# Kernel tuning notes

Hardware: AMD Instinct MI355X
Metric: run time of the kernel (lower is better)

Reference implementation:

```python
import jax, jax.numpy as jnp
import numpy as np

NT, NS, NH, NG = 365, 1024, 64, 32
NW = NH * 8 + 2


def setup_inputs() -> dict:
    key = jax.random.key(0)
    k1, k2, k3, k4 = jax.random.split(key, 4)
    std = 1.0 / np.sqrt(NH)
    x = jax.random.normal(k1, (NT, NS, 4), dtype=jnp.float32)
    # make P (precip) nonnegative and T1 < T2 plausible-ish; math is still generic
    xc = jax.random.normal(k2, (NS, NG), dtype=jnp.float32)
    fc_w = jax.random.uniform(k3, (NW, NG), minval=-std, maxval=std, dtype=jnp.float32)
    fc_b = jax.random.uniform(k4, (NW,), minval=-std, maxval=std, dtype=jnp.float32)
    return {"x": x, "xc": xc, "fc_w": fc_w, "fc_b": fc_b}


def reference(x, xc, fc_w, fc_b):
    nh = NH
    P, E, T1, T2 = x[..., 0], x[..., 1], x[..., 2], x[..., 3]  # each [nt, ns]
    Ta = (T1 + T2) * 0.5
    # rain/snow partition: rP = 1 - arccos((T1+T2)/(T2-T1))/3.1415, masked
    valid = (T1 < 0) & (T2 > 0)
    denom = jnp.where(valid, T2 - T1, 1.0)
    ratio = jnp.clip(jnp.where(valid, (T1 + T2) / denom, 0.0), -0.999999, 0.999999)
    rP = 1.0 - jnp.arccos(ratio) / 3.1415
    rP = jnp.where(T1 >= 0, 1.0, rP)
    rP = jnp.where(T2 <= 0, 0.0, rP)
    Ps = (1.0 - rP) * P  # snow   [nt, ns]
    Pl = rP * P          # liquid [nt, ns]

    w = xc @ fc_w.T + fc_b  # [ns, nh*8+2]
    gm = jnp.exp(w[:, :nh]) + 1.0
    ge = jax.nn.sigmoid(w[:, nh:2 * nh]) * 2.0
    go = jax.nn.sigmoid(w[:, 2 * nh:3 * nh])
    gl = jnp.exp(w[:, 3 * nh:4 * nh] * 2.0)
    ga = jax.nn.softmax(w[:, 4 * nh:5 * nh], axis=1)  # Dropout in eval mode = identity
    gb = jax.nn.sigmoid(w[:, 5 * nh:6 * nh])
    qb = jax.nn.relu(w[:, -1]) / nh  # [ns]
    kb = jax.nn.sigmoid(w[:, 6 * nh:7 * nh]) / 10.0
    gi = jax.nn.sigmoid(w[:, 7 * nh:8 * nh])

    ns = P.shape[1]
    init = (jnp.zeros((ns, nh), jnp.float32),) * 3  # S0, H0, G0

    def step(carry, inp):
        S0, H0, G0 = carry
        Ps_k, Pl_k, Ta_k, E_k = inp  # each [ns]
        S = S0 + Ps_k[:, None]
        Sm = jnp.minimum(S0, jax.nn.relu(Ta_k[:, None] * gm))  # snowmelt
        H = jax.nn.relu(H0 + Sm + Pl_k[:, None] * gi - E_k[:, None] * ge)
        Q1 = jax.nn.relu(H - gl)
        Q2a = jnp.minimum(H, gl) * go
        Q2 = Q2a * (1.0 - gb)
        G = G0 + Q2a * gb
        Q3 = G * kb
        H0n = jnp.minimum(H - Q2a, gl)
        G0n = G - Q3
        S0n = S - Sm
        Y = jnp.sum((Q1 + Q2 + Q3 + qb[:, None]) * ga, axis=1)  # [ns]
        return (S0n, H0n, G0n), Y

    _, Yout = jax.lax.scan(step, init, (Ps, Pl, Ta, E))
    return Yout  # [nt, ns]
```

## Files before the change

kernel.cpp:

```cpp
#include <hip/hip_runtime.h>
#include <math.h>

#define NT_ 365
#define NS_ 1024
#define NH_ 64
#define NG_ 32
#define NW_ 514
#define CH_ 64
#define NCHUNK_ 6
#define YPAD_ 65
#define SUB_ 8

__device__ __forceinline__ float sigmoidf(float v) {
  return 1.0f / (1.0f + expf(-v));
}

__device__ __forceinline__ float4 compute_met(float4 xv) {
  const float P = xv.x, E = xv.y, T1 = xv.z, T2 = xv.w;
  const float Ta = (T1 + T2) * 0.5f;
  float rP;
  if (T2 <= 0.0f) {
    rP = 0.0f;
  } else if (T1 >= 0.0f) {
    rP = 1.0f;
  } else {
    float r = (T1 + T2) / (T2 - T1);
    r = fminf(fmaxf(r, -0.999999f), 0.999999f);
    rP = 1.0f - acosf(r) * (1.0f / 3.1415f);
  }
  float4 m;
  m.x = (1.0f - rP) * P;
  m.y = rP * P;
  m.z = fmaxf(Ta, 0.0f);
  m.w = E;
  return m;
}

__global__ __launch_bounds__(256) void waternet_scan(
    const float* __restrict__ x,
    const float* __restrict__ xc,
    const float* __restrict__ fc_w,
    const float* __restrict__ fc_b,
    float* __restrict__ out)
{
  __shared__ float4 smet[4][CH_];
  __shared__ float  ytile[4][CH_ * YPAD_];

  const int tid  = threadIdx.x;
  const int lane = tid & 63;
  const int wv   = tid >> 6;
  const int site = (blockIdx.x << 2) + wv;
  const int us   = __builtin_amdgcn_readfirstlane(site);
  const float4* xp = (const float4*)x;

  float4 xcur = xp[lane * NS_ + site];

  float acc[8];
#pragma unroll
  for (int k = 0; k < 8; ++k) acc[k] = fc_b[k * NH_ + lane];
  float accq = fc_b[NW_ - 1];

  const float4* xcq = (const float4*)(xc + us * NG_);
  const float4* wq4 = (const float4*)fc_w;
#pragma unroll
  for (int g4 = 0; g4 < NG_ / 4; ++g4) {
    const float4 xv = xcq[g4];
#pragma unroll
    for (int k = 0; k < 8; ++k) {
      const float4 w = wq4[(k * NH_ + lane) * (NG_ / 4) + g4];
      acc[k] = fmaf(xv.x, w.x, acc[k]);
      acc[k] = fmaf(xv.y, w.y, acc[k]);
      acc[k] = fmaf(xv.z, w.z, acc[k]);
      acc[k] = fmaf(xv.w, w.w, acc[k]);
    }
    {
      const float4 w = wq4[(NW_ - 1) * (NG_ / 4) + g4];
      accq = fmaf(xv.x, w.x, accq);
      accq = fmaf(xv.y, w.y, accq);
      accq = fmaf(xv.z, w.z, accq);
      accq = fmaf(xv.w, w.w, accq);
    }
  }

  const float gm = expf(acc[0]) + 1.0f;
  const float ge = sigmoidf(acc[1]) * 2.0f;
  const float go = sigmoidf(acc[2]);
  const float gl = expf(acc[3] * 2.0f);
  float mx = acc[4];
#pragma unroll
  for (int mm = 32; mm >= 1; mm >>= 1) mx = fmaxf(mx, __shfl_xor(mx, mm, 64));
  const float ex = expf(acc[4] - mx);
  float sm = ex;
#pragma unroll
  for (int mm = 32; mm >= 1; mm >>= 1) sm += __shfl_xor(sm, mm, 64);
  const float ga = ex / sm;
  const float gb = sigmoidf(acc[5]);
  const float kb = sigmoidf(acc[6]) * 0.1f;
  const float gi = sigmoidf(acc[7]);
  const float qb = fmaxf(accq, 0.0f) * (1.0f / NH_);
  const float kb1m = 1.0f - kb;
  const float nge  = -ge;
  const float gq1  = go * (1.0f - gb) - 1.0f;

  float S0 = 0.0f, H0 = 0.0f, G0 = 0.0f;

  smet[wv][lane] = compute_met(xcur);

  auto step = [&](const float4 mt, float* ywaddr) {
    const float melt = mt.z * gm;
    const float Sm   = fminf(S0, melt);
    const float base = H0 + Sm;
    S0 = (S0 - Sm) + mt.x;
    const float t3 = fmaf(mt.y, gi, base);
    const float H  = fmaxf(fmaf(mt.w, nge, t3), 0.0f);
    const float M  = fminf(H, gl);
    const float Q2a = M * go;
    H0 = fminf(H - Q2a, gl);
    const float G = fmaf(Q2a, gb, G0);
    G0 = G * kb1m;
    *ywaddr = fmaf(G, kb, fmaf(M, gq1, H)) * ga;
  };

  float*       yw = &ytile[wv][lane];
  const float* yr = &ytile[wv][lane * YPAD_];

#pragma unroll 1
  for (int c = 0; c < NCHUNK_; ++c) {
    int tn = (c + 1) * CH_ + lane;
    tn = (tn < NT_) ? tn : (NT_ - 1);
    const float4 xnext = xp[tn * NS_ + site];

    const float4* mp = &smet[wv][0];

    float4 mb0[SUB_], mb1[SUB_];
#pragma unroll
    for (int u = 0; u < SUB_; ++u) mb0[u] = mp[u];

#pragma unroll
    for (int sc = 0; sc < CH_ / SUB_; ++sc) {
      float4*       cur = (sc & 1) ? mb1 : mb0;
      float4*       nxt = (sc & 1) ? mb0 : mb1;
      if (sc < CH_ / SUB_ - 1) {
#pragma unroll
        for (int u = 0; u < SUB_; ++u) nxt[u] = mp[SUB_ * (sc + 1) + u];
      }
#pragma unroll
      for (int u = 0; u < SUB_; ++u)
        step(cur[u], yw + (SUB_ * sc + u) * YPAD_);
    }

    float r0 = 0.0f, r1 = 0.0f, r2 = 0.0f, r3 = 0.0f;
#pragma unroll
    for (int h = 0; h < CH_; h += 4) {
      r0 += yr[h + 0];
      r1 += yr[h + 1];
      r2 += yr[h + 2];
      r3 += yr[h + 3];
    }
    const int t_out = c * CH_ + lane;
    if (t_out < NT_) out[t_out * NS_ + site] = ((r0 + r1) + (r2 + r3)) + qb;

    if (c + 1 < NCHUNK_) smet[wv][lane] = compute_met(xnext);
  }
}

extern "C" void kernel_launch(void* const* d_in, const int* in_sizes, int n_in,
                              void* d_out, int out_size, void* d_ws, size_t ws_size,
                              hipStream_t stream) {
  const float* x    = (const float*)d_in[0];
  const float* xc   = (const float*)d_in[1];
  const float* fc_w = (const float*)d_in[2];
  const float* fc_b = (const float*)d_in[3];
  float* out = (float*)d_out;

  hipLaunchKernelGGL(waternet_scan, dim3(NS_ / 4), dim3(256), 0, stream,
                     x, xc, fc_w, fc_b, out);
}
```

Measured before the change: 87.52 us.

## Split recurrence into producer/consumer wavefronts pipelined through shared memory

The serial scan is split into two halves. Two wavefronts run the S/H recurrence for two sites each and write the pre-clamp value z to a double-buffered LDS array. The other two wavefronts run the G recurrence and the output accumulation one phase behind, and also load the next phase's met data. This shortens the per-step dependency chain that each wavefront carries, so the two halves overlap across phases. In exchange it adds a block-wide barrier every 32 steps, LDS traffic for z, and uses setprio on the producer waves.

New measurement: 94.74 us. 8.2% more time.

```diff
diff --git a/kernel.cpp b/kernel.cpp
--- a/kernel.cpp
+++ b/kernel.cpp
@@ -6,10 +6,10 @@
 #define NH_ 64
 #define NG_ 32
 #define NW_ 514
+#define PH_ 32
+#define NPH_ 12
 #define CH_ 64
-#define NCHUNK_ 6
 #define YPAD_ 65
-#define SUB_ 8
 
 __device__ __forceinline__ float sigmoidf(float v) {
   return 1.0f / (1.0f + expf(-v));
@@ -43,125 +43,244 @@
     const float* __restrict__ fc_b,
     float* __restrict__ out)
 {
-  __shared__ float4 smet[4][CH_];
+  __shared__ float  zbuf[2][4][PH_][NH_];
+  __shared__ float4 metb[2][4][PH_];
   __shared__ float  ytile[4][CH_ * YPAD_];
 
   const int tid  = threadIdx.x;
   const int lane = tid & 63;
   const int wv   = tid >> 6;
-  const int site = (blockIdx.x << 2) + wv;
-  const int us   = __builtin_amdgcn_readfirstlane(site);
-  const float4* xp = (const float4*)x;
-
-  float4 xcur = xp[lane * NS_ + site];
-
-  float acc[8];
-#pragma unroll
-  for (int k = 0; k < 8; ++k) acc[k] = fc_b[k * NH_ + lane];
-  float accq = fc_b[NW_ - 1];
-
-  const float4* xcq = (const float4*)(xc + us * NG_);
+  const bool isA = (wv < 2);
+  const int s0   = (wv & 1) * 2;
+  const int s1   = s0 + 1;
+  const int base = blockIdx.x << 2;
+  const int site0 = base + s0, site1 = base + s1;
+  const float4* xp  = (const float4*)x;
   const float4* wq4 = (const float4*)fc_w;
-#pragma unroll
-  for (int g4 = 0; g4 < NG_ / 4; ++g4) {
-    const float4 xv = xcq[g4];
-#pragma unroll
-    for (int k = 0; k < 8; ++k) {
-      const float4 w = wq4[(k * NH_ + lane) * (NG_ / 4) + g4];
-      acc[k] = fmaf(xv.x, w.x, acc[k]);
-      acc[k] = fmaf(xv.y, w.y, acc[k]);
-      acc[k] = fmaf(xv.z, w.z, acc[k]);
-      acc[k] = fmaf(xv.w, w.w, acc[k]);
+  const int us0 = __builtin_amdgcn_readfirstlane(site0);
+  const float4* xcq0 = (const float4*)(xc + us0 * NG_);
+  const float4* xcq1 = (const float4*)(xc + (us0 + 1) * NG_);
+
+  float gm0=0,nge0=0,gi0=0,mgo0=0,glA0=0,S0a=0,H0a=0;
+  float gm1=0,nge1=0,gi1=0,mgo1=0,glA1=0,S0b=0,H0b=0;
+  float glB0=0,kb1m0=0,cgb0=0,c10=0,ga0=0,qb0=0,Gh0=0;
+  float glB1=0,kb1m1=0,cgb1=0,c11=0,ga1=0,qb1=0,Gh1=0;
+
+  const int mslot = s0 + (lane >> 5);
+  const int msite = base + mslot;
+  const int mt    = lane & 31;
+
+  if (isA) {
+    float a0[5], a1[5];
+    const int rows[5] = {0, 1, 2, 3, 7};
+#pragma unroll
+    for (int k = 0; k < 5; ++k) { a0[k] = fc_b[rows[k]*NH_ + lane]; a1[k] = a0[k]; }
+#pragma unroll
+    for (int g4 = 0; g4 < NG_/4; ++g4) {
+      const float4 x0 = xcq0[g4];
+      const float4 x1 = xcq1[g4];
+#pragma unroll
+      for (int k = 0; k < 5; ++k) {
+        const float4 w = wq4[(rows[k]*NH_ + lane)*(NG_/4) + g4];
+        a0[k]=fmaf(x0.x,w.x,a0[k]); a0[k]=fmaf(x0.y,w.y,a0[k]);
+        a0[k]=fmaf(x0.z,w.z,a0[k]); a0[k]=fmaf(x0.w,w.w,a0[k]);
+        a1[k]=fmaf(x1.x,w.x,a1[k]); a1[k]=fmaf(x1.y,w.y,a1[k]);
+        a1[k]=fmaf(x1.z,w.z,a1[k]); a1[k]=fmaf(x1.w,w.w,a1[k]);
+      }
+    }
+    gm0=expf(a0[0])+1.f; nge0=-2.f*sigmoidf(a0[1]); mgo0=-sigmoidf(a0[2]);
+    glA0=expf(a0[3]*2.f); gi0=sigmoidf(a0[4]);
+    gm1=expf(a1[0])+1.f; nge1=-2.f*sigmoidf(a1[1]); mgo1=-sigmoidf(a1[2]);
+    glA1=expf(a1[3]*2.f); gi1=sigmoidf(a1[4]);
+    __builtin_amdgcn_s_setprio(1);
+  } else {
+    float4 xv0m = xp[mt * NS_ + msite];
+    float a0[5], a1[5];
+    const int rows[5] = {2, 3, 4, 5, 6};
+#pragma unroll
+    for (int k = 0; k < 5; ++k) { a0[k] = fc_b[rows[k]*NH_ + lane]; a1[k] = a0[k]; }
+    float aq0 = fc_b[NW_-1], aq1 = aq0;
+#pragma unroll
+    for (int g4 = 0; g4 < NG_/4; ++g4) {
+      const float4 x0 = xcq0[g4];
+      const float4 x1 = xcq1[g4];
+#pragma unroll
+      for (int k = 0; k < 5; ++k) {
+        const float4 w = wq4[(rows[k]*NH_ + lane)*(NG_/4) + g4];
+        a0[k]=fmaf(x0.x,w.x,a0[k]); a0[k]=fmaf(x0.y,w.y,a0[k]);
+        a0[k]=fmaf(x0.z,w.z,a0[k]); a0[k]=fmaf(x0.w,w.w,a0[k]);
+        a1[k]=fmaf(x1.x,w.x,a1[k]); a1[k]=fmaf(x1.y,w.y,a1[k]);
+        a1[k]=fmaf(x1.z,w.z,a1[k]); a1[k]=fmaf(x1.w,w.w,a1[k]);
+      }
+      {
+        const float4 w = wq4[(NW_-1)*(NG_/4) + g4];
+        aq0=fmaf(x0.x,w.x,aq0); aq0=fmaf(x0.y,w.y,aq0);
+        aq0=fmaf(x0.z,w.z,aq0); aq0=fmaf(x0.w,w.w,aq0);
+        aq1=fmaf(x1.x,w.x,aq1); aq1=fmaf(x1.y,w.y,aq1);
+        aq1=fmaf(x1.z,w.z,aq1); aq1=fmaf(x1.w,w.w,aq1);
+      }
     }
     {
-      const float4 w = wq4[(NW_ - 1) * (NG_ / 4) + g4];
-      accq = fmaf(xv.x, w.x, accq);
-      accq = fmaf(xv.y, w.y, accq);
-      accq = fmaf(xv.z, w.z, accq);
-      accq = fmaf(xv.w, w.w, accq);
-    }
+      const float go = sigmoidf(a0[0]);
+      glB0 = expf(a0[1]*2.f);
+      float mx = a0[2];
+#pragma unroll
+      for (int m2=32;m2>=1;m2>>=1) mx = fmaxf(mx, __shfl_xor(mx,m2,64));
+      const float ex = expf(a0[2]-mx);
+      float sm = ex;
+#pragma unroll
+      for (int m2=32;m2>=1;m2>>=1) sm += __shfl_xor(sm,m2,64);
+      ga0 = ex/sm;
+      const float gb = sigmoidf(a0[3]);
+      const float kb = 0.1f*sigmoidf(a0[4]);
+      qb0 = fmaxf(aq0,0.f)*(1.f/NH_);
+      kb1m0 = 1.f-kb; cgb0 = ga0*kb*gb*go; c10 = ga0*(go*(1.f-gb)-1.f);
+    }
+    {
+      const float go = sigmoidf(a1[0]);
+      glB1 = expf(a1[1]*2.f);
+      float mx = a1[2];
+#pragma unroll
+      for (int m2=32;m2>=1;m2>>=1) mx = fmaxf(mx, __shfl_xor(mx,m2,64));
+      const float ex = expf(a1[2]-mx);
+      float sm = ex;
+#pragma unroll
+      for (int m2=32;m2>=1;m2>>=1) sm += __shfl_xor(sm,m2,64);
+      ga1 = ex/sm;
+      const float gb = sigmoidf(a1[3]);
+      const float kb = 0.1f*sigmoidf(a1[4]);
+      qb1 = fmaxf(aq1,0.f)*(1.f/NH_);
+      kb1m1 = 1.f-kb; cgb1 = ga1*kb*gb*go; c11 = ga1*(go*(1.f-gb)-1.f);
+    }
+    metb[0][mslot][mt] = compute_met(xv0m);
   }
 
-  const float gm = expf(acc[0]) + 1.0f;
-  const float ge = sigmoidf(acc[1]) * 2.0f;
-  const float go = sigmoidf(acc[2]);
-  const float gl = expf(acc[3] * 2.0f);
-  float mx = acc[4];
-#pragma unroll
-  for (int mm = 32; mm >= 1; mm >>= 1) mx = fmaxf(mx, __shfl_xor(mx, mm, 64));
-  const float ex = expf(acc[4] - mx);
-  float sm = ex;
-#pragma unroll
-  for (int mm = 32; mm >= 1; mm >>= 1) sm += __shfl_xor(sm, mm, 64);
-  const float ga = ex / sm;
-  const float gb = sigmoidf(acc[5]);
-  const float kb = sigmoidf(acc[6]) * 0.1f;
-  const float gi = sigmoidf(acc[7]);
-  const float qb = fmaxf(accq, 0.0f) * (1.0f / NH_);
-  const float kb1m = 1.0f - kb;
-  const float nge  = -ge;
-  const float gq1  = go * (1.0f - gb) - 1.0f;
-
-  float S0 = 0.0f, H0 = 0.0f, G0 = 0.0f;
-
-  smet[wv][lane] = compute_met(xcur);
-
-  auto step = [&](const float4 mt, float* ywaddr) {
-    const float melt = mt.z * gm;
-    const float Sm   = fminf(S0, melt);
-    const float base = H0 + Sm;
-    S0 = (S0 - Sm) + mt.x;
-    const float t3 = fmaf(mt.y, gi, base);
-    const float H  = fmaxf(fmaf(mt.w, nge, t3), 0.0f);
-    const float M  = fminf(H, gl);
-    const float Q2a = M * go;
-    H0 = fminf(H - Q2a, gl);
-    const float G = fmaf(Q2a, gb, G0);
-    G0 = G * kb1m;
-    *ywaddr = fmaf(G, kb, fmaf(M, gq1, H)) * ga;
+  auto produceA = [&](int p) {
+    const int pb = p & 1;
+    float4 ma[8], mb[8], na[8], nb[8];
+#pragma unroll
+    for (int i=0;i<8;++i){ ma[i]=metb[pb][s0][i]; mb[i]=metb[pb][s1][i]; }
+#pragma unroll
+    for (int g=0; g<4; ++g) {
+      float4* cA=(g&1)?na:ma; float4* cB=(g&1)?nb:mb;
+      float4* nA=(g&1)?ma:na; float4* nB=(g&1)?mb:nb;
+      if (g<3) {
+#pragma unroll
+        for (int i=0;i<8;++i){
+          nA[i]=metb[pb][s0][(g+1)*8+i];
+          nB[i]=metb[pb][s1][(g+1)*8+i];
+        }
+      }
+#pragma unroll
+      for (int u=0; u<8; ++u) {
+        const int uu = g*8+u;
+        {
+          const float4 m = cA[u];
+          const float melt = m.z*gm0;
+          const float Sm   = fminf(S0a, melt);
+          const float tS   = S0a + m.x;
+          S0a = tS - Sm;
+          const float d = fmaf(m.y, gi0, fmaf(m.w, nge0, Sm));
+          const float z = H0a + d;
+          zbuf[pb][s0][uu][lane] = z;
+          const float Hh = fmaxf(z, 0.f);
+          const float M  = __builtin_amdgcn_fmed3f(z, 0.f, glA0);
+          H0a = fminf(fmaf(mgo0, M, Hh), glA0);
+        }
+        {
+          const float4 m = cB[u];
+          const float melt = m.z*gm1;
+          const float Sm   = fminf(S0b, melt);
+          const float tS   = S0b + m.x;
+          S0b = tS - Sm;
+          const float d = fmaf(m.y, gi1, fmaf(m.w, nge1, Sm));
+          const float z = H0b + d;
+          zbuf[pb][s1][uu][lane] = z;
+          const float Hh = fmaxf(z, 0.f);
+          const float M  = __builtin_amdgcn_fmed3f(z, 0.f, glA1);
+          H0b = fminf(fmaf(mgo1, M, Hh), glA1);
+        }
+      }
+    }
   };
 
-  float*       yw = &ytile[wv][lane];
-  const float* yr = &ytile[wv][lane * YPAD_];
+  auto consumeB = [&](int q) {
+    const int qb2 = q & 1;
+    const int tb  = qb2 * PH_;
+    float za[8], zb[8], wa[8], wb[8];
+#pragma unroll
+    for (int i=0;i<8;++i){ za[i]=zbuf[qb2][s0][i][lane]; zb[i]=zbuf[qb2][s1][i][lane]; }
+#pragma unroll
+    for (int g=0; g<4; ++g) {
+      float* cA=(g&1)?wa:za; float* cB=(g&1)?wb:zb;
+      float* nA=(g&1)?za:wa; float* nB=(g&1)?zb:wb;
+      if (g<3) {
+#pragma unroll
+        for (int i=0;i<8;++i){
+          nA[i]=zbuf[qb2][s0][(g+1)*8+i][lane];
+          nB[i]=zbuf[qb2][s1][(g+1)*8+i][lane];
+        }
+      }
+#pragma unroll
+      for (int u=0; u<8; ++u) {
+        const int tl = tb + g*8 + u;
+        {
+          const float z  = cA[u];
+          const float Hh = fmaxf(z, 0.f);
+          const float M  = __builtin_amdgcn_fmed3f(z, 0.f, glB0);
+          Gh0 = fmaf(kb1m0, Gh0, cgb0*M);
+          ytile[s0][tl*YPAD_ + lane] = Gh0 + fmaf(c10, M, ga0*Hh);
+        }
+        {
+          const float z  = cB[u];
+          const float Hh = fmaxf(z, 0.f);
+          const float M  = __builtin_amdgcn_fmed3f(z, 0.f, glB1);
+          Gh1 = fmaf(kb1m1, Gh1, cgb1*M);
+          ytile[s1][tl*YPAD_ + lane] = Gh1 + fmaf(c11, M, ga1*Hh);
+        }
+      }
+    }
+  };
+
+  auto reduceB = [&](int c) {
+    const float* y0 = &ytile[s0][lane*YPAD_];
+    const float* y1 = &ytile[s1][lane*YPAD_];
+    float r0=0,r1=0,r2=0,r3=0, t0=0,t1=0,t2=0,t3=0;
+#pragma unroll
+    for (int h=0; h<CH_; h+=4) {
+      r0+=y0[h]; r1+=y0[h+1]; r2+=y0[h+2]; r3+=y0[h+3];
+      t0+=y1[h]; t1+=y1[h+1]; t2+=y1[h+2]; t3+=y1[h+3];
+    }
+    const int t_out = c*CH_ + lane;
+    if (t_out < NT_) {
+      out[t_out*NS_ + site0] = ((r0+r1)+(r2+r3)) + qb0;
+      out[t_out*NS_ + site1] = ((t0+t1)+(t2+t3)) + qb1;
+    }
+  };
+
+  __syncthreads();
 
 #pragma unroll 1
-  for (int c = 0; c < NCHUNK_; ++c) {
-    int tn = (c + 1) * CH_ + lane;
-    tn = (tn < NT_) ? tn : (NT_ - 1);
-    const float4 xnext = xp[tn * NS_ + site];
-
-    const float4* mp = &smet[wv][0];
-
-    float4 mb0[SUB_], mb1[SUB_];
-#pragma unroll
-    for (int u = 0; u < SUB_; ++u) mb0[u] = mp[u];
-
-#pragma unroll
-    for (int sc = 0; sc < CH_ / SUB_; ++sc) {
-      float4*       cur = (sc & 1) ? mb1 : mb0;
-      float4*       nxt = (sc & 1) ? mb0 : mb1;
-      if (sc < CH_ / SUB_ - 1) {
-#pragma unroll
-        for (int u = 0; u < SUB_; ++u) nxt[u] = mp[SUB_ * (sc + 1) + u];
-      }
-#pragma unroll
-      for (int u = 0; u < SUB_; ++u)
-        step(cur[u], yw + (SUB_ * sc + u) * YPAD_);
-    }
-
-    float r0 = 0.0f, r1 = 0.0f, r2 = 0.0f, r3 = 0.0f;
-#pragma unroll
-    for (int h = 0; h < CH_; h += 4) {
-      r0 += yr[h + 0];
-      r1 += yr[h + 1];
-      r2 += yr[h + 2];
-      r3 += yr[h + 3];
-    }
-    const int t_out = c * CH_ + lane;
-    if (t_out < NT_) out[t_out * NS_ + site] = ((r0 + r1) + (r2 + r3)) + qb;
-
-    if (c + 1 < NCHUNK_) smet[wv][lane] = compute_met(xnext);
+  for (int p = 0; p < NPH_; ++p) {
+    if (isA) {
+      produceA(p);
+    } else {
+      float4 xvm = make_float4(0.f,0.f,0.f,0.f);
+      const bool hm = (p + 1 < NPH_);
+      if (hm) {
+        int tg = PH_*(p+1) + mt;
+        if (tg > NT_-1) tg = NT_-1;
+        xvm = xp[tg*NS_ + msite];
+      }
+      if (p > 0) {
+        consumeB(p-1);
+        if ((p-1) & 1) reduceB((p-1) >> 1);
+      }
+      if (hm) metb[(p+1)&1][mslot][mt] = compute_met(xvm);
+    }
+    __syncthreads();
   }
+  if (!isA) { consumeB(NPH_-1); reduceB((NPH_-1) >> 1); }
 }
 
 extern "C" void kernel_launch(void* const* d_in, const int* in_sizes, int n_in,
```
